# Kernel tuning notes

Hardware: AMD Instinct MI355X
Metric: run time of the kernel (lower is better)

## Reference

```python
import jax, jax.numpy as jnp
import numpy as np

NEG_INF = -1e30
DEN_SCALE = 1.0  # den_scale from init


def segment_logsumexp(scores, segids, num_segments):
    """Numerically stable logsumexp of `scores` grouped by `segids`."""
    m = jax.ops.segment_max(scores, segids, num_segments=num_segments)
    m_safe = jnp.where(m > NEG_INF / 2, m, 0.0)
    s = jax.ops.segment_sum(jnp.exp(scores - m_safe[segids]), segids,
                            num_segments=num_segments)
    return jnp.where(s > 0, jnp.log(s) + m_safe, NEG_INF)


def fsa_log_marginal(ll, seqlen, arc_src, arc_dst, arc_pdf, arc_w,
                     init_logp, final_logp):
    """Forward (alpha) recursion over a compiled FSA.
    ll: [T, C] pdf log-likelihoods; arcs: [A]; states: [S].
    Returns scalar log total path probability."""
    S = init_logp.shape[0]

    def step(carry, ll_t):
        alpha, t = carry
        # score of each arc taken at frame t
        scores = alpha[arc_src] + arc_w + ll_t[arc_pdf]  # [A]
        new_alpha = segment_logsumexp(scores, arc_dst, S)  # [S]
        # freeze alpha once past this sequence's length
        alpha = jnp.where(t < seqlen, new_alpha, alpha)
        return (alpha, t + 1), None

    (alpha, _), _ = jax.lax.scan(step, (init_logp, jnp.array(0, jnp.int32)), ll)
    return jax.nn.logsumexp(alpha + final_logp)


# batched numerator: per-utterance FSA topology ([B, A_num] arc arrays)
_num_marginal = jax.vmap(fsa_log_marginal,
                         in_axes=(0, 0, 0, 0, 0, 0, None, None))
# batched denominator: shared FSA topology ([A_den] arc arrays)
_den_marginal = jax.vmap(fsa_log_marginal,
                         in_axes=(0, 0, None, None, None, None, None, None))


def setup_inputs() -> dict:
    key = jax.random.key(0)
    ks = jax.random.split(key, 10)
    B, T, C = 16, 500, 3000
    S_den, A_den_rand = 2000, 46000
    L = 250  # numerator chain emission length (<= min seqlen)
    S_num = L + 1

    inp = jax.random.normal(ks[0], (B, T, C), dtype=jnp.float32)
    # log-softmax-like normalization, as pdf log-likelihoods would be
    inp = jax.nn.log_softmax(inp, axis=-1)
    seqlengths = jax.random.randint(ks[1], (B,), 300, T + 1).astype(jnp.int32)

    # ---- numerator FSAs: left-to-right chain + self-loops, per utterance ----
    fwd_src = jnp.arange(L, dtype=jnp.int32)            # i -> i+1
    fwd_dst = fwd_src + 1
    loop = jnp.arange(S_num, dtype=jnp.int32)           # self-loops on all states
    num_arc_src = jnp.broadcast_to(jnp.concatenate([fwd_src, loop]), (B, L + S_num))
    num_arc_dst = jnp.broadcast_to(jnp.concatenate([fwd_dst, loop]), (B, L + S_num))
    num_arc_pdf = jax.random.randint(ks[2], (B, L + S_num), 0, C).astype(jnp.int32)
    num_arc_w = jnp.zeros((B, L + S_num), dtype=jnp.float32)
    num_init_logp = jnp.full((S_num,), NEG_INF, jnp.float32).at[0].set(0.0)
    num_final_logp = jnp.full((S_num,), NEG_INF, jnp.float32).at[S_num - 1].set(0.0)

    # ---- denominator FSA: random phone-LM-like graph + self-loops ----
    rnd_src = jax.random.randint(ks[3], (A_den_rand,), 0, S_den)
    rnd_dst = jax.random.randint(ks[4], (A_den_rand,), 0, S_den)
    loops = jnp.arange(S_den)
    den_arc_src = jnp.concatenate([rnd_src, loops]).astype(jnp.int32)
    den_arc_dst = jnp.concatenate([rnd_dst, loops]).astype(jnp.int32)
    A_den = den_arc_src.shape[0]
    den_arc_pdf = jax.random.randint(ks[5], (A_den,), 0, C).astype(jnp.int32)
    den_arc_w = 0.1 * jax.random.normal(ks[6], (A_den,), dtype=jnp.float32)
    den_init_logp = jnp.full((S_den,), NEG_INF, jnp.float32).at[0].set(0.0)
    den_final_logp = jnp.zeros((S_den,), dtype=jnp.float32)

    return {
        "input": inp, "seqlengths": seqlengths,
        "num_arc_src": num_arc_src, "num_arc_dst": num_arc_dst,
        "num_arc_pdf": num_arc_pdf, "num_arc_w": num_arc_w,
        "num_init_logp": num_init_logp, "num_final_logp": num_final_logp,
        "den_arc_src": den_arc_src, "den_arc_dst": den_arc_dst,
        "den_arc_pdf": den_arc_pdf, "den_arc_w": den_arc_w,
        "den_init_logp": den_init_logp, "den_final_logp": den_final_logp,
    }


def reference(input, seqlengths, num_arc_src, num_arc_dst, num_arc_pdf,
              num_arc_w, num_init_logp, num_final_logp, den_arc_src,
              den_arc_dst, den_arc_pdf, den_arc_w, den_init_logp,
              den_final_logp):
    num_llh = _num_marginal(input, seqlengths, num_arc_src, num_arc_dst,
                            num_arc_pdf, num_arc_w, num_init_logp,
                            num_final_logp)
    den_llh = _den_marginal(input, seqlengths, den_arc_src, den_arc_dst,
                            den_arc_pdf, den_arc_w, den_init_logp,
                            den_final_logp)
    loss = -(num_llh - DEN_SCALE * den_llh)
    return loss.sum()
```

## Files before the change

kernel.cpp:

```cpp
#include <hip/hip_runtime.h>

#define NEG_INF_F (-1e30f)
#define MAX_S 2048
#define MAX_C 3008
#define NCH   128

#define VB_SIZE 8216
#define EL_COPY 3016
#define EL_BUF  6032
#define EL_SIZE 12064


__global__ void zero_kernel(int* __restrict__ p, int n) {
  int i = blockIdx.x * blockDim.x + threadIdx.x;
  if (i < n) p[i] = 0;
}

__global__ void hist_kernel(const int* __restrict__ dst, int A, int A_stride,
                            int* __restrict__ cnt, int S) {
  int b = blockIdx.y;
  int i = blockIdx.x * blockDim.x + threadIdx.x;
  if (i < A) atomicAdd(&cnt[b * S + dst[(size_t)b * A_stride + i]], 1);
}

__global__ void hist_chunk_kernel(const int* __restrict__ dst, int A, int chunk, int S,
                                  int* __restrict__ hist) {
  int c = blockIdx.x;
  int i1 = min(A, (c + 1) * chunk);
  for (int i = c * chunk + threadIdx.x; i < i1; i += blockDim.x)
    atomicAdd(&hist[c * S + dst[i]], 1);
}

__global__ void colsum_kernel(const int* __restrict__ hist, int nch, int S,
                              int* __restrict__ cnt) {
  int s = blockIdx.x * blockDim.x + threadIdx.x;
  if (s < S) {
    int t = 0;
    for (int c = 0; c < nch; ++c) t += hist[c * S + s];
    cnt[s] = t;
  }
}

__global__ __launch_bounds__(1024)
void rank_perm_kernel(const int* __restrict__ cnt, int S,
                      int* __restrict__ perm, int* __restrict__ invperm) {
  __shared__ int c[2048];
  __shared__ int R[2048];
  const int tid = threadIdx.x;
  for (int i = tid; i < 2048; i += 1024) c[i] = (i < S) ? cnt[i] : -1;
  __syncthreads();
  for (int u = 0; u < 2; ++u) {
    int s = tid + u * 1024;
    if (s < S) {
      int cs = c[s], r = 0;
      for (int j = 0; j < S; ++j) {
        int cj = c[j];
        r += (cj > cs) || (cj == cs && j < s);
      }
      R[r] = s;
    }
  }
  __syncthreads();
  for (int u = 0; u < 2; ++u) {
    int slot = tid + u * 1024;
    if (slot < S) {
      int state = (slot < 1024) ? R[slot] : R[S - 1 - (slot - 1024)];
      perm[slot] = state;
      invperm[state] = slot;
    }
  }
}

__global__ void pc_kernel(const int* __restrict__ cnt, const int* __restrict__ perm,
                          int S, int* __restrict__ pc) {
  int slot = blockIdx.x * blockDim.x + threadIdx.x;
  if (slot < 2048) pc[slot] = (slot < S) ? ((cnt[perm[slot]] + 3) & ~3) : 0;
}

__global__ void padcnt_kernel(const int* __restrict__ cnt, int n, int* __restrict__ out) {
  int i = blockIdx.x * blockDim.x + threadIdx.x;
  if (i < n) out[i] = (cnt[i] + 3) & ~3;
}

__global__ __launch_bounds__(1024) void scan_kernel(const int* __restrict__ cnt,
                                                    int* __restrict__ rp, int S) {
  __shared__ int buf[2][2048];
  const int tid = threadIdx.x;
  const int b = blockIdx.x;
  const int* c = cnt + (size_t)b * S;
  int* r = rp + (size_t)b * (S + 1);
  for (int u = 0; u < 2; ++u) {
    int i = tid + u * 1024;
    buf[0][i] = (i < S) ? c[i] : 0;
  }
  __syncthreads();
  int cur = 0;
  for (int off = 1; off < 2048; off <<= 1) {
    for (int u = 0; u < 2; ++u) {
      int i = tid + u * 1024;
      buf[cur ^ 1][i] = buf[cur][i] + ((i >= off) ? buf[cur][i - off] : 0);
    }
    __syncthreads();
    cur ^= 1;
  }
  for (int u = 0; u < 2; ++u) {
    int i = tid + u * 1024;
    if (i <= S) r[i] = (i == 0) ? 0 : buf[cur][i - 1];
  }
  if (tid == 0) r[S] = buf[cur][S - 1];
}

__global__ void off_perm_kernel(int* __restrict__ hist, int nch, int S,
                                const int* __restrict__ rp, const int* __restrict__ perm) {
  int slot = blockIdx.x * blockDim.x + threadIdx.x;
  if (slot < S) {
    int state = perm[slot];
    int run = rp[slot];
    for (int c = 0; c < nch; ++c) {
      int h = hist[c * S + state];
      hist[c * S + state] = run;
      run += h;
    }
  }
}

__global__ void pad_den_kernel(const int* __restrict__ rp, const int* __restrict__ cnt,
                               const int* __restrict__ perm, int S, int C,
                               uint2* __restrict__ meta) {
  int slot = blockIdx.x * blockDim.x + threadIdx.x;
  if (slot < S) {
    int p = rp[slot] + cnt[perm[slot]];
    int e = rp[slot + 1];
    const int pc = min(slot, C - 1);
    uint2 pad = make_uint2((unsigned)(slot * 4) | ((unsigned)(pc * 4) << 16), 0u);
    for (; p < e; ++p) meta[p] = pad;
  }
}

__global__ void fill_chunk_kernel(const int* __restrict__ src, const int* __restrict__ dst,
                                  const int* __restrict__ pdf, const float* __restrict__ w,
                                  int A, int chunk, int S, int* __restrict__ hoff,
                                  const int* __restrict__ inv, uint2* __restrict__ meta) {
  int c = blockIdx.y;
  int s = blockIdx.x * blockDim.x + threadIdx.x;
  if (s >= S) return;
  int i1 = min(A, (c + 1) * chunk);
  int p = hoff[c * S + s];
  for (int i = c * chunk; i < i1; ++i) {
    if (dst[i] == s) {
      meta[p++] = make_uint2((unsigned)(inv[src[i]] * 4) | ((unsigned)(pdf[i] * 4) << 16),
                             __float_as_uint(__expf(w[i])));
    }
  }
}

__global__ void fill_kernel(const int* __restrict__ src, const int* __restrict__ dst,
                            const int* __restrict__ pdf, const float* __restrict__ w,
                            int A, int A_stride, const int* __restrict__ rp, int S,
                            uint2* __restrict__ meta, int meta_stride) {
  int b = blockIdx.y;
  int s = blockIdx.x * blockDim.x + threadIdx.x;
  if (s >= S) return;
  const int*   sb = src + (size_t)b * A_stride;
  const int*   db = dst + (size_t)b * A_stride;
  const int*   pb = pdf + (size_t)b * A_stride;
  const float* wb = w   + (size_t)b * A_stride;
  const int*   rpb = rp + (size_t)b * (S + 1);
  uint2* mb = meta + (size_t)b * meta_stride;
  int p = rpb[s];
  for (int i = 0; i < A; ++i) {
    if (db[i] == s) {
      mb[p++] = make_uint2((unsigned)sb[i] | ((unsigned)pb[i] << 16), __float_as_uint(wb[i]));
    }
  }
  uint2 pad = make_uint2(0u, __float_as_uint(NEG_INF_F));
  int e = rpb[s + 1];
  for (; p < e; ++p) mb[p] = pad;
}

__global__ __launch_bounds__(1024)
void wave_desc_kernel(const int* __restrict__ rp, int cap4, int* __restrict__ desc) {
  __shared__ int wm[32];
  const int tid = threadIdx.x;
  const int w = tid >> 6;
  int cA = (rp[tid + 1] - rp[tid]) >> 2;
  int sB = 2047 - tid;
  int cB = (rp[sB + 1] - rp[sB]) >> 2;
  for (int off = 32; off; off >>= 1) {
    cA = max(cA, __shfl_down(cA, off));
    cB = max(cB, __shfl_down(cB, off));
  }
  if ((tid & 63) == 0) { wm[w] = cA; wm[16 + w] = cB; }
  __syncthreads();
  if (tid == 0) {
    int off = 0;
    for (int i = 0; i < 16; ++i) { desc[i] = off; off += wm[i] * 128; }
    for (int i = 0; i < 16; ++i) { desc[16 + i] = off; off += wm[16 + i] * 128; }
    for (int i = 0; i < 16; ++i) { desc[32 + i] = wm[i]; desc[48 + i] = wm[16 + i]; }
    desc[64] = (off <= cap4) ? 1 : 0;
    desc[65] = off;
  }
}

__global__ __launch_bounds__(64)
void repack_choice_kernel(const uint2* __restrict__ meta, const int* __restrict__ rp,
                          const int* __restrict__ desc, int C, uint2* __restrict__ ilv) {
  if (!desc[64]) return;
  const int w = blockIdx.x & 15;
  const bool isB = blockIdx.x >= 16;
  const int l = threadIdx.x;
  const int base4 = desc[(isB ? 16 : 0) + w];
  const int wmax  = desc[(isB ? 48 : 32) + w];
  const int P = wmax * 4;
  if (P == 0) return;

  const int slot_l = isB ? (2047 - (w * 64 + l)) : (w * 64 + l);
  const int r0_l = rp[slot_l];
  const int n_l  = rp[slot_l + 1] - r0_l;
  const int pc_l = min(slot_l, C - 1);
  const uint2 pad_l = make_uint2((unsigned)(slot_l * 4) | ((unsigned)(pc_l * 4) << 16), 0u);

  if (P > 64) {
    const int n4 = n_l >> 2;
    for (int c = 0; c < wmax; ++c) {
      for (int part = 0; part < 2; ++part) {
        int u4 = base4 + c * 128 + part * 64 + l;
        uint2 v0 = pad_l, v1 = pad_l;
        if (c < n4) {
          v0 = meta[r0_l + 4 * c + 2 * part];
          v1 = meta[r0_l + 4 * c + 2 * part + 1];
        }
        ilv[2 * u4]     = v0;
        ilv[2 * u4 + 1] = v1;
      }
    }
    return;
  }

  __shared__ uint2 sp[64][65];

  for (int p = 0; p < P; ++p)
    sp[l][p] = (p < n_l) ? meta[r0_l + p] : pad_l;
  __syncthreads();

  if (l < P) {
    unsigned long long cs[4]  = {0, 0, 0, 0};
    unsigned long long cp2[4] = {0, 0, 0, 0};
    for (int r = 0; r < 64; ++r) {
      uint2 a = sp[r][l];
      unsigned srcoff = a.x & 0xFFFFu;
      unsigned pdfoff = a.x >> 16;
      const int b0 = (int)((srcoff >> 2) & 31u);
      int bestk = 0, bestc = 256;
#pragma unroll
      for (int k = 0; k < 4; ++k) {
        int bb = (b0 + 8 * k) & 31;
        int c = (int)((cs[bb >> 3] >> ((bb & 7) * 8)) & 0xFFull);
        if (c < bestc) { bestc = c; bestk = k; }
      }
      const int bs = (b0 + 8 * bestk) & 31;
      cs[bs >> 3] += (1ULL << ((bs & 7) * 8));
      const int q0 = (int)((pdfoff >> 2) & 31u);
      const int q1 = (q0 + 8) & 31;
      const int c0 = (int)((cp2[q0 >> 3] >> ((q0 & 7) * 8)) & 0xFFull);
      const int c1 = (int)((cp2[q1 >> 3] >> ((q1 & 7) * 8)) & 0xFFull);
      const int bj = (c1 < c0) ? 1 : 0;
      const int qb = bj ? q1 : q0;
      cp2[qb >> 3] += (1ULL << ((qb & 7) * 8));
      a.x = (srcoff + (unsigned)bestk * 8224u) | ((pdfoff + (unsigned)bj * 12064u) << 16);
      sp[r][l] = a;
    }
  }
  __syncthreads();

  for (int c = 0; c < wmax; ++c) {
    for (int part = 0; part < 2; ++part) {
      int u4 = base4 + c * 128 + part * 64 + l;
      ilv[2 * u4]     = sp[l][4 * c + 2 * part];
      ilv[2 * u4 + 1] = sp[l][4 * c + 2 * part + 1];
    }
  }
}


__device__ __forceinline__ float row_lse(const uint2* __restrict__ meta, int k, int e,
                                         const float* __restrict__ alpha,
                                         const float* __restrict__ lcur) {
  float mm0 = NEG_INF_F, ss0 = 0.0f, mm1 = NEG_INF_F, ss1 = 0.0f;
  const int n4 = (e - k) >> 2;
  const uint4* p = (const uint4*)(meta + k);
  if (n4 > 0) {
    uint4 A = p[0], Bv = p[1];
    float t0 = alpha[A.x & 0xFFFFu] + __uint_as_float(A.y) + lcur[A.x >> 16];
    float t1 = alpha[A.z & 0xFFFFu] + __uint_as_float(A.w) + lcur[A.z >> 16];
    float t2 = alpha[Bv.x & 0xFFFFu] + __uint_as_float(Bv.y) + lcur[Bv.x >> 16];
    float t3 = alpha[Bv.z & 0xFFFFu] + __uint_as_float(Bv.w) + lcur[Bv.z >> 16];
    for (int c2 = 1; c2 < n4; ++c2) {
      uint4 A2 = p[2 * c2], B2 = p[2 * c2 + 1];
      float u0 = alpha[A2.x & 0xFFFFu] + __uint_as_float(A2.y) + lcur[A2.x >> 16];
      float u1 = alpha[A2.z & 0xFFFFu] + __uint_as_float(A2.w) + lcur[A2.z >> 16];
      float u2 = alpha[B2.x & 0xFFFFu] + __uint_as_float(B2.y) + lcur[B2.x >> 16];
      float u3 = alpha[B2.z & 0xFFFFu] + __uint_as_float(B2.w) + lcur[B2.z >> 16];
      float mc = fmaxf(fmaxf(t0, t1), fmaxf(t2, t3));
      if ((c2 & 1) != 0) {
        float nm = fmaxf(mm0, mc);
        ss0 = ss0 * __expf(mm0 - nm) +
              ((__expf(t0 - nm) + __expf(t1 - nm)) + (__expf(t2 - nm) + __expf(t3 - nm)));
        mm0 = nm;
      } else {
        float nm = fmaxf(mm1, mc);
        ss1 = ss1 * __expf(mm1 - nm) +
              ((__expf(t0 - nm) + __expf(t1 - nm)) + (__expf(t2 - nm) + __expf(t3 - nm)));
        mm1 = nm;
      }
      t0 = u0; t1 = u1; t2 = u2; t3 = u3;
    }
    float mc = fmaxf(fmaxf(t0, t1), fmaxf(t2, t3));
    if ((n4 & 1) != 0) {
      float nm = fmaxf(mm0, mc);
      ss0 = ss0 * __expf(mm0 - nm) +
            ((__expf(t0 - nm) + __expf(t1 - nm)) + (__expf(t2 - nm) + __expf(t3 - nm)));
      mm0 = nm;
    } else {
      float nm = fmaxf(mm1, mc);
      ss1 = ss1 * __expf(mm1 - nm) +
            ((__expf(t0 - nm) + __expf(t1 - nm)) + (__expf(t2 - nm) + __expf(t3 - nm)));
      mm1 = nm;
    }
  }
  float nm = fmaxf(mm0, mm1);
  float ssc = ss0 * __expf(mm0 - nm) + ss1 * __expf(mm1 - nm);
  return (ssc > 0.0f) ? (__logf(ssc) + nm) : NEG_INF_F;
}

__device__ __forceinline__ void stage_row(const float* __restrict__ row,
                                          float* __restrict__ lds, int C, int tid, int nt) {
  if (((C & 3) == 0) && ((((uintptr_t)row) & 15) == 0)) {
    const float4* r4 = (const float4*)row;
    const int n = C >> 2;
    for (int i = tid; i < n; i += nt) ((float4*)lds)[i] = r4[i];
  } else {
    for (int i = tid; i < C; i += nt) lds[i] = row[i];
  }
}

__device__ __forceinline__ float ldsF(const float* base, unsigned boff) {
  return *(const float*)((const char*)base + boff);
}

#define ACC4(X, Y, s0, s1, s2, s3)                                                         \
  s0 = fmaf(__uint_as_float((X).y), ldsF(vbuf, (X).x & 0xFFFFu) * ldsF(el, (X).x >> 16), s0); \
  s1 = fmaf(__uint_as_float((X).w), ldsF(vbuf, (X).z & 0xFFFFu) * ldsF(el, (X).z >> 16), s1); \
  s2 = fmaf(__uint_as_float((Y).y), ldsF(vbuf, (Y).x & 0xFFFFu) * ldsF(el, (Y).x >> 16), s2); \
  s3 = fmaf(__uint_as_float((Y).w), ldsF(vbuf, (Y).z & 0xFFFFu) * ldsF(el, (Y).z >> 16), s3);

__global__ __launch_bounds__(1024, 1)
void fsa_forward_lin(const float* __restrict__ ll, const int* __restrict__ seqlen,
                     const uint2* __restrict__ den_meta, const uint4* __restrict__ den_ilv,
                     const int* __restrict__ den_desc,
                     const int* __restrict__ den_rp, const int* __restrict__ den_perm, int S_den,
                     const uint2* __restrict__ num_meta, const int* __restrict__ num_rp,
                     int num_stride, int S_num,
                     const float* __restrict__ den_init, const float* __restrict__ den_final,
                     const float* __restrict__ num_init, const float* __restrict__ num_final,
                     int T, int C, int B, float* __restrict__ out_llh)
{
  __shared__ float alpha[MAX_S];
  __shared__ float vbuf[VB_SIZE];
  __shared__ float elbuf[EL_SIZE];
  __shared__ float red[16];
  __shared__ int   sdesc[66];

  const int tid = threadIdx.x;
  const int nt  = 1024;
  const bool is_den = ((int)blockIdx.x) < B;
  const int b = is_den ? (int)blockIdx.x : ((int)blockIdx.x - B);
  const int S = is_den ? S_den : S_num;
  const float* fin  = is_den ? den_final : num_final;
  const int*   perm = is_den ? den_perm  : nullptr;

  const int L = seqlen[b];
  const float* llb = ll + ((size_t)b * T) * C;

  if (is_den) {
    for (int i = tid; i < 66; i += nt) sdesc[i] = den_desc[i];

    const int w = tid >> 6, l = tid & 63;
    const int slotA = tid;
    const int slotB = 2047 - tid;
    const int rA0 = den_rp[slotA], rA1 = den_rp[slotA + 1];
    const int rB0 = den_rp[slotB], rB1 = den_rp[slotB + 1];
    float a0 = (slotA < S) ? den_init[den_perm[slotA]] : NEG_INF_F;
    float a1 = (slotB < S) ? den_init[den_perm[slotB]] : NEG_INF_F;

    const int nvec = C >> 2;
    const bool pf = ((C & 3) == 0) && ((((uintptr_t)llb) & 15) == 0) &&
                    (nvec <= nt) && (C <= MAX_C);

    float lm = fmaxf(a0, a1);
    for (int off = 32; off; off >>= 1) lm = fmaxf(lm, __shfl_down(lm, off));
    if ((tid & 63) == 0) red[tid >> 6] = lm;
    if (L > 0) {
      if (pf) {
        if (tid < nvec) {
          float4 r = ((const float4*)llb)[tid];
          float4 e = make_float4(__expf(r.x), __expf(r.y), __expf(r.z), __expf(r.w));
          ((float4*)elbuf)[tid] = e;
          ((float4*)(elbuf + EL_COPY))[tid] = e;
        }
      } else {
        for (int i = tid; i < C; i += nt) {
          float e = __expf(llb[i]);
          elbuf[i] = e;
          elbuf[i + EL_COPY] = e;
        }
      }
    }
    __syncthreads();
    float M = red[0];
#pragma unroll
    for (int i = 1; i < 16; ++i) M = fmaxf(M, red[i]);

    const bool ilv_ok = sdesc[64] != 0;
    const uint4* pA4 = den_ilv + sdesc[w] + l;
    const uint4* pB4 = den_ilv + sdesc[16 + w] + l;
    const int nA = sdesc[32 + w], nB = sdesc[48 + w];

    int cur = 0;
    for (int t = 0; t < L; ++t) {
      {
        float va = __expf(a0 - M), vb = __expf(a1 - M);
        vbuf[slotA] = va; vbuf[slotA + 2056] = va;
        vbuf[slotA + 4112] = va; vbuf[slotA + 6168] = va;
        vbuf[slotB] = vb; vbuf[slotB + 2056] = vb;
        vbuf[slotB + 4112] = vb; vbuf[slotB + 6168] = vb;
      }
      __syncthreads();

      const float* el = elbuf + (cur ? EL_BUF : 0);

      float4 nx;
      const bool donx = pf && (t + 1 < L) && (tid < nvec);
      if (donx) nx = ((const float4*)(llb + (size_t)(t + 1) * C))[tid];

      float sA0 = 0, sA1 = 0, sA2 = 0, sA3 = 0;
      float sB0 = 0, sB1 = 0, sB2 = 0, sB3 = 0;
      if (ilv_ok) {
        if (nA > 0) {
          uint4 X0 = pA4[0], Y0 = pA4[64];
          if (nA > 1) {
            uint4 X1 = pA4[128], Y1 = pA4[192];
            for (int c = 2; c < nA; ++c) {
              uint4 X2 = pA4[c * 128], Y2 = pA4[c * 128 + 64];
              ACC4(X0, Y0, sA0, sA1, sA2, sA3);
              X0 = X1; Y0 = Y1; X1 = X2; Y1 = Y2;
            }
            ACC4(X0, Y0, sA0, sA1, sA2, sA3);
            X0 = X1; Y0 = Y1;
          }
          ACC4(X0, Y0, sA0, sA1, sA2, sA3);
        }
        if (nB > 0) {
          uint4 X0 = pB4[0], Y0 = pB4[64];
          for (int c = 1; c < nB; ++c) {
            uint4 X1 = pB4[c * 128], Y1 = pB4[c * 128 + 64];
            ACC4(X0, Y0, sB0, sB1, sB2, sB3);
            X0 = X1; Y0 = Y1;
          }
          ACC4(X0, Y0, sB0, sB1, sB2, sB3);
        }
      } else {
        const uint4* pA = (const uint4*)(den_meta + rA0);
        const uint4* pB = (const uint4*)(den_meta + rB0);
        const int nAr = (rA1 - rA0) >> 2, nBr = (rB1 - rB0) >> 2;
        const int n = nAr > nBr ? nAr : nBr;
        for (int c = 0; c < n; ++c) {
          if (c < nAr) {
            uint4 X = pA[2 * c], Y = pA[2 * c + 1];
            ACC4(X, Y, sA0, sA1, sA2, sA3);
          }
          if (c < nBr) {
            uint4 X = pB[2 * c], Y = pB[2 * c + 1];
            ACC4(X, Y, sB0, sB1, sB2, sB3);
          }
        }
      }
      float sA = (sA0 + sA1) + (sA2 + sA3);
      float sB = (sB0 + sB1) + (sB2 + sB3);

      a0 = (sA > 0.0f) ? (__logf(sA) + M) : NEG_INF_F;
      a1 = (sB > 0.0f) ? (__logf(sB) + M) : NEG_INF_F;

      float* eln = elbuf + (cur ? 0 : EL_BUF);
      if (donx) {
        float4 e = make_float4(__expf(nx.x), __expf(nx.y), __expf(nx.z), __expf(nx.w));
        ((float4*)eln)[tid] = e;
        ((float4*)(eln + EL_COPY))[tid] = e;
      } else if (!pf && t + 1 < L) {
        const float* nr = llb + (size_t)(t + 1) * C;
        for (int i = tid; i < C; i += nt) {
          float e = __expf(nr[i]);
          eln[i] = e;
          eln[i + EL_COPY] = e;
        }
      }

      float lm2 = fmaxf(a0, a1);
      for (int off = 32; off; off >>= 1) lm2 = fmaxf(lm2, __shfl_down(lm2, off));
      if ((tid & 63) == 0) red[tid >> 6] = lm2;
      __syncthreads();
      M = red[0];
#pragma unroll
      for (int i = 1; i < 16; ++i) M = fmaxf(M, red[i]);
      cur ^= 1;
    }
    alpha[slotA] = a0;
    alpha[slotB] = a1;
    __syncthreads();
  } else {
    const uint2* meta = num_meta + (size_t)b * num_stride;
    const int*   rp   = num_rp + (size_t)b * (S_num + 1);
    for (int s = tid; s < MAX_S; s += nt) alpha[s] = (s < S) ? num_init[s] : NEG_INF_F;
    int rs[2] = {0, 0}, re[2] = {0, 0};
    for (int u = 0; u < 2; ++u) {
      int s = tid + u * nt;
      if (s < S) { rs[u] = rp[s]; re[u] = rp[s + 1]; }
    }
    __syncthreads();
    for (int t = 0; t < L; ++t) {
      stage_row(llb + (size_t)t * C, elbuf, C, tid, nt);
      __syncthreads();
      float nv[2];
      for (int u = 0; u < 2; ++u) {
        int s = tid + u * nt;
        nv[u] = (s < S) ? row_lse(meta, rs[u], re[u], alpha, elbuf) : NEG_INF_F;
      }
      __syncthreads();
      for (int u = 0; u < 2; ++u) {
        int s = tid + u * nt;
        if (s < S) alpha[s] = nv[u];
      }
      __syncthreads();
    }
  }

  float lm = -3.0e38f;
  for (int s = tid; s < S; s += nt) lm = fmaxf(lm, alpha[s] + fin[perm ? perm[s] : s]);
  for (int off = 32; off; off >>= 1) lm = fmaxf(lm, __shfl_down(lm, off));
  if ((tid & 63) == 0) red[tid >> 6] = lm;
  __syncthreads();
  if (tid < 64) {
    float v = (tid < 16) ? red[tid] : -3.0e38f;
    for (int off = 32; off; off >>= 1) v = fmaxf(v, __shfl_down(v, off));
    if (tid == 0) red[0] = v;
  }
  __syncthreads();
  const float M = red[0];

  float ls = 0.0f;
  for (int s = tid; s < S; s += nt) ls += __expf(alpha[s] + fin[perm ? perm[s] : s] - M);
  for (int off = 32; off; off >>= 1) ls += __shfl_down(ls, off);
  __syncthreads();
  if ((tid & 63) == 0) red[tid >> 6] = ls;
  __syncthreads();
  if (tid < 64) {
    float v = (tid < 16) ? red[tid] : 0.0f;
    for (int off = 32; off; off >>= 1) v += __shfl_down(v, off);
    if (tid == 0) out_llh[(is_den ? 0 : B) + b] = __logf(v) + M;
  }
}


__device__ __forceinline__ unsigned enc_f(float x) {
  unsigned u = __float_as_uint(x);
  return u ^ (unsigned)(((int)u >> 31) | 0x80000000);
}
__device__ __forceinline__ float dec_f(unsigned e) {
  unsigned mask = ((int)e >= 0) ? 0xFFFFFFFFu : 0x80000000u;
  return __uint_as_float(e ^ mask);
}

__global__ __launch_bounds__(1024)
void fsa_forward_fallback(
    const float* __restrict__ ll, const int* __restrict__ seqlen,
    const int* __restrict__ den_src, const int* __restrict__ den_dst,
    const int* __restrict__ den_pdf, const float* __restrict__ den_w,
    int A_den, const float* __restrict__ den_init, const float* __restrict__ den_final, int S_den,
    const int* __restrict__ num_src, const int* __restrict__ num_dst,
    const int* __restrict__ num_pdf, const float* __restrict__ num_w,
    int A_num, const float* __restrict__ num_init, const float* __restrict__ num_final, int S_num,
    int T, int C, int B, float* __restrict__ out_llh)
{
  __shared__ float    alpha[MAX_S];
  __shared__ unsigned menc[MAX_S];
  __shared__ float    msafe[MAX_S];
  __shared__ float    ssum[MAX_S];
  __shared__ float    llrow[MAX_C];

  const int tid = threadIdx.x;
  const int nt  = blockDim.x;
  const bool is_den = ((int)blockIdx.x) < B;
  const int b = is_den ? (int)blockIdx.x : ((int)blockIdx.x - B);
  const int S = is_den ? S_den : S_num;
  const int A = is_den ? A_den : A_num;
  const float* init = is_den ? den_init  : num_init;
  const float* fin  = is_den ? den_final : num_final;
  const int*   asrc = is_den ? den_src  : (num_src + (size_t)b * A_num);
  const int*   adst = is_den ? den_dst  : (num_dst + (size_t)b * A_num);
  const int*   apdf = is_den ? den_pdf  : (num_pdf + (size_t)b * A_num);
  const float* aw   = is_den ? den_w    : (num_w   + (size_t)b * A_num);

  for (int s = tid; s < S; s += nt) { alpha[s] = init[s]; menc[s] = 0u; ssum[s] = 0.0f; }
  __syncthreads();

  const int L = seqlen[b];
  const float* llb = ll + ((size_t)b * T) * C;

  for (int t = 0; t < L; ++t) {
    const float* row = llb + (size_t)t * C;
    for (int i = tid; i < C; i += nt) llrow[i] = row[i];
    __syncthreads();
    for (int i = tid; i < A; i += nt) {
      float score = alpha[asrc[i]] + aw[i] + llrow[apdf[i]];
      atomicMax(&menc[adst[i]], enc_f(score));
    }
    __syncthreads();
    for (int s = tid; s < S; s += nt) {
      float m = dec_f(menc[s]);
      msafe[s] = (m > -5e29f) ? m : 0.0f;
    }
    __syncthreads();
    for (int i = tid; i < A; i += nt) {
      int d = adst[i];
      float score = alpha[asrc[i]] + aw[i] + llrow[apdf[i]];
      atomicAdd(&ssum[d], __expf(score - msafe[d]));
    }
    __syncthreads();
    for (int s = tid; s < S; s += nt) {
      float sum = ssum[s];
      alpha[s] = (sum > 0.0f) ? (__logf(sum) + msafe[s]) : NEG_INF_F;
      menc[s] = 0u; ssum[s] = 0.0f;
    }
    __syncthreads();
  }

  float lm = -3.0e38f;
  for (int s = tid; s < S; s += nt) lm = fmaxf(lm, alpha[s] + fin[s]);
  for (int off = 32; off; off >>= 1) lm = fmaxf(lm, __shfl_down(lm, off));
  const int nwaves = nt >> 6;
  if ((tid & 63) == 0) msafe[tid >> 6] = lm;
  __syncthreads();
  if (tid < 64) {
    float v = (tid < nwaves) ? msafe[tid] : -3.0e38f;
    for (int off = 32; off; off >>= 1) v = fmaxf(v, __shfl_down(v, off));
    if (tid == 0) msafe[MAX_S - 1] = v;
  }
  __syncthreads();
  const float M = msafe[MAX_S - 1];
  float ls = 0.0f;
  for (int s = tid; s < S; s += nt) ls += __expf(alpha[s] + fin[s] - M);
  for (int off = 32; off; off >>= 1) ls += __shfl_down(ls, off);
  if ((tid & 63) == 0) ssum[tid >> 6] = ls;
  __syncthreads();
  if (tid < 64) {
    float v = (tid < nwaves) ? ssum[tid] : 0.0f;
    for (int off = 32; off; off >>= 1) v += __shfl_down(v, off);
    if (tid == 0) out_llh[(is_den ? 0 : B) + b] = __logf(v) + M;
  }
}

__global__ void final_loss_kernel(const float* __restrict__ llh, int B, float* __restrict__ out) {
  int lane = threadIdx.x;
  float v = (lane < B) ? (llh[lane] - llh[B + lane]) : 0.0f;
  for (int off = 32; off; off >>= 1) v += __shfl_down(v, off);
  if (lane == 0) out[0] = v;
}

extern "C" void kernel_launch(void* const* d_in, const int* in_sizes, int n_in,
                              void* d_out, int out_size, void* d_ws, size_t ws_size,
                              hipStream_t stream) {
  const float* ll        = (const float*)d_in[0];
  const int*   seqlen    = (const int*)  d_in[1];
  const int*   num_src   = (const int*)  d_in[2];
  const int*   num_dst   = (const int*)  d_in[3];
  const int*   num_pdf   = (const int*)  d_in[4];
  const float* num_w     = (const float*)d_in[5];
  const float* num_init  = (const float*)d_in[6];
  const float* num_final = (const float*)d_in[7];
  const int*   den_src   = (const int*)  d_in[8];
  const int*   den_dst   = (const int*)  d_in[9];
  const int*   den_pdf   = (const int*)  d_in[10];
  const float* den_w     = (const float*)d_in[11];
  const float* den_init  = (const float*)d_in[12];
  const float* den_final = (const float*)d_in[13];

  const int B     = in_sizes[1];
  const int A_num = in_sizes[2] / B;
  const int S_num = in_sizes[6];
  const int A_den = in_sizes[8];
  const int S_den = in_sizes[12];
  const int T     = 500;
  const int C     = in_sizes[0] / (B * T);

  const int den_cap    = A_den + 3 * S_den + 64;
  const int num_stride = A_num + 3 * S_num + 64;
  const int cap4       = den_cap + 32768;

  size_t off = 0;
  auto alloc = [&](size_t bytes, size_t align) -> size_t {
    off = (off + align - 1) / align * align;
    size_t r = off; off += bytes; return r;
  };
  size_t o_den_meta = alloc((size_t)den_cap * 8, 16);
  size_t o_den_ilv  = alloc((size_t)cap4 * 16, 16);
  size_t o_desc     = alloc((size_t)66 * 4, 4);
  size_t o_num_meta = alloc((size_t)B * num_stride * 8, 16);
  size_t o_den_rp   = alloc((size_t)2049 * 4, 4);
  size_t o_num_rp   = alloc((size_t)B * (S_num + 1) * 4, 4);
  size_t o_den_cnt  = alloc((size_t)S_den * 4, 4);
  size_t o_perm     = alloc((size_t)2048 * 4, 4);
  size_t o_inv      = alloc((size_t)S_den * 4, 4);
  size_t o_pc       = alloc((size_t)2048 * 4, 4);
  size_t o_num_pc   = alloc((size_t)B * S_num * 4, 4);
  size_t o_hist     = alloc((size_t)NCH * S_den * 4, 4);
  size_t o_num_cnt  = alloc((size_t)B * S_num * 4, 4);
  size_t o_llh      = alloc((size_t)2 * B * 4, 4);
  const bool use_csr = (off <= ws_size) && (S_den >= 1) && (S_den <= 2048) &&
                       (S_num >= 1) && (S_num <= 2048) && (C <= MAX_C) && (C >= 1);

  char* wsb = (char*)d_ws;
  float* llh = (float*)(wsb + (use_csr ? o_llh : 0));

  if (use_csr) {
    uint2* den_meta = (uint2*)(wsb + o_den_meta);
    uint4* den_ilv  = (uint4*)(wsb + o_den_ilv);
    int*   desc     = (int*)(wsb + o_desc);
    uint2* num_meta = (uint2*)(wsb + o_num_meta);
    int*   den_rp   = (int*)(wsb + o_den_rp);
    int*   num_rp   = (int*)(wsb + o_num_rp);
    int*   den_cnt  = (int*)(wsb + o_den_cnt);
    int*   perm     = (int*)(wsb + o_perm);
    int*   inv      = (int*)(wsb + o_inv);
    int*   pc       = (int*)(wsb + o_pc);
    int*   num_pc   = (int*)(wsb + o_num_pc);
    int*   hist     = (int*)(wsb + o_hist);
    int*   num_cnt  = (int*)(wsb + o_num_cnt);

    const int chunk = (A_den + NCH - 1) / NCH;

    int ztot = NCH * S_den + B * S_num;
    zero_kernel<<<(ztot + 255) / 256, 256, 0, stream>>>(hist, ztot);

    hist_chunk_kernel<<<NCH, 256, 0, stream>>>(den_dst, A_den, chunk, S_den, hist);
    hist_kernel<<<dim3((A_num + 255) / 256, B), 256, 0, stream>>>(num_dst, A_num, A_num,
                                                                  num_cnt, S_num);

    colsum_kernel<<<(S_den + 255) / 256, 256, 0, stream>>>(hist, NCH, S_den, den_cnt);
    rank_perm_kernel<<<1, 1024, 0, stream>>>(den_cnt, S_den, perm, inv);
    pc_kernel<<<8, 256, 0, stream>>>(den_cnt, perm, S_den, pc);
    scan_kernel<<<1, 1024, 0, stream>>>(pc, den_rp, 2048);
    wave_desc_kernel<<<1, 1024, 0, stream>>>(den_rp, cap4, desc);

    padcnt_kernel<<<(B * S_num + 255) / 256, 256, 0, stream>>>(num_cnt, B * S_num, num_pc);
    scan_kernel<<<B, 1024, 0, stream>>>(num_pc, num_rp, S_num);

    off_perm_kernel<<<(S_den + 255) / 256, 256, 0, stream>>>(hist, NCH, S_den, den_rp, perm);
    pad_den_kernel<<<(S_den + 255) / 256, 256, 0, stream>>>(den_rp, den_cnt, perm, S_den, C,
                                                            den_meta);
    fill_chunk_kernel<<<dim3((S_den + 255) / 256, NCH), 256, 0, stream>>>(
        den_src, den_dst, den_pdf, den_w, A_den, chunk, S_den, hist, inv, den_meta);
    fill_kernel<<<dim3((S_num + 255) / 256, B), 256, 0, stream>>>(
        num_src, num_dst, num_pdf, num_w, A_num, A_num, num_rp, S_num, num_meta, num_stride);

    repack_choice_kernel<<<32, 64, 0, stream>>>(den_meta, den_rp, desc, C, (uint2*)den_ilv);

    fsa_forward_lin<<<2 * B, 1024, 0, stream>>>(
        ll, seqlen, den_meta, den_ilv, desc, den_rp, perm, S_den,
        num_meta, num_rp, num_stride, S_num,
        den_init, den_final, num_init, num_final, T, C, B, llh);
  } else {
    fsa_forward_fallback<<<2 * B, 1024, 0, stream>>>(
        ll, seqlen,
        den_src, den_dst, den_pdf, den_w, A_den, den_init, den_final, S_den,
        num_src, num_dst, num_pdf, num_w, A_num, num_init, num_final, S_num,
        T, C, B, llh);
  }

  final_loss_kernel<<<1, 64, 0, stream>>>(llh, B, (float*)d_out);
}
```

Before: 2.900 ms.

## Fuse graph preprocessing kernels to cut launch count

Merges the denominator histogram, rank/permutation, padded-count scan and wave descriptor steps into one single-block kernel that uses shared-memory atomics. Also fuses the numerator histogram, scan and fill into one per-utterance kernel, and folds zeroing into the chunk histogram. The goal is to remove about ten small kernel launches and their global round trips from the preprocessing chain. The cost is that the denominator histogram now runs serially in a single block over all arcs, and the numerator scan runs on a single thread.

Result: no change. 2.861 ms (-1.3%).

```diff
diff --git a/kernel.cpp b/kernel.cpp
--- a/kernel.cpp
+++ b/kernel.cpp
@@ -11,50 +11,38 @@
 #define EL_SIZE 12064
 
 
-__global__ void zero_kernel(int* __restrict__ p, int n) {
-  int i = blockIdx.x * blockDim.x + threadIdx.x;
-  if (i < n) p[i] = 0;
-}
-
-__global__ void hist_kernel(const int* __restrict__ dst, int A, int A_stride,
-                            int* __restrict__ cnt, int S) {
-  int b = blockIdx.y;
-  int i = blockIdx.x * blockDim.x + threadIdx.x;
-  if (i < A) atomicAdd(&cnt[b * S + dst[(size_t)b * A_stride + i]], 1);
-}
-
 __global__ void hist_chunk_kernel(const int* __restrict__ dst, int A, int chunk, int S,
                                   int* __restrict__ hist) {
-  int c = blockIdx.x;
+  const int c = blockIdx.x;
+  int* h = hist + (size_t)c * S;
+  for (int i = threadIdx.x; i < S; i += blockDim.x) h[i] = 0;
+  __syncthreads();
   int i1 = min(A, (c + 1) * chunk);
   for (int i = c * chunk + threadIdx.x; i < i1; i += blockDim.x)
-    atomicAdd(&hist[c * S + dst[i]], 1);
-}
-
-__global__ void colsum_kernel(const int* __restrict__ hist, int nch, int S,
-                              int* __restrict__ cnt) {
-  int s = blockIdx.x * blockDim.x + threadIdx.x;
-  if (s < S) {
-    int t = 0;
-    for (int c = 0; c < nch; ++c) t += hist[c * S + s];
-    cnt[s] = t;
-  }
+    atomicAdd(&h[dst[i]], 1);
 }
 
 __global__ __launch_bounds__(1024)
-void rank_perm_kernel(const int* __restrict__ cnt, int S,
-                      int* __restrict__ perm, int* __restrict__ invperm) {
-  __shared__ int c[2048];
+void den_stats_kernel(const int* __restrict__ dst, int A, int S, int cap4,
+                      int* __restrict__ rp_g, int* __restrict__ perm_g,
+                      int* __restrict__ inv_g, int* __restrict__ cnt_g,
+                      int* __restrict__ desc) {
+  __shared__ int cnt[2048];
   __shared__ int R[2048];
+  __shared__ int P2[2048];
+  __shared__ int buf[2][2048];
+  __shared__ int wm[32];
   const int tid = threadIdx.x;
-  for (int i = tid; i < 2048; i += 1024) c[i] = (i < S) ? cnt[i] : -1;
+  for (int i = tid; i < 2048; i += 1024) cnt[i] = 0;
+  __syncthreads();
+  for (int i = tid; i < A; i += 1024) atomicAdd(&cnt[dst[i]], 1);
   __syncthreads();
   for (int u = 0; u < 2; ++u) {
     int s = tid + u * 1024;
     if (s < S) {
-      int cs = c[s], r = 0;
+      int cs = cnt[s], r = 0;
       for (int j = 0; j < S; ++j) {
-        int cj = c[j];
+        int cj = cnt[j];
         r += (cj > cs) || (cj == cs && j < s);
       }
       R[r] = s;
@@ -63,36 +51,12 @@
   __syncthreads();
   for (int u = 0; u < 2; ++u) {
     int slot = tid + u * 1024;
-    if (slot < S) {
-      int state = (slot < 1024) ? R[slot] : R[S - 1 - (slot - 1024)];
-      perm[slot] = state;
-      invperm[state] = slot;
-    }
-  }
-}
-
-__global__ void pc_kernel(const int* __restrict__ cnt, const int* __restrict__ perm,
-                          int S, int* __restrict__ pc) {
-  int slot = blockIdx.x * blockDim.x + threadIdx.x;
-  if (slot < 2048) pc[slot] = (slot < S) ? ((cnt[perm[slot]] + 3) & ~3) : 0;
-}
-
-__global__ void padcnt_kernel(const int* __restrict__ cnt, int n, int* __restrict__ out) {
-  int i = blockIdx.x * blockDim.x + threadIdx.x;
-  if (i < n) out[i] = (cnt[i] + 3) & ~3;
-}
-
-__global__ __launch_bounds__(1024) void scan_kernel(const int* __restrict__ cnt,
-                                                    int* __restrict__ rp, int S) {
-  __shared__ int buf[2][2048];
-  const int tid = threadIdx.x;
-  const int b = blockIdx.x;
-  const int* c = cnt + (size_t)b * S;
-  int* r = rp + (size_t)b * (S + 1);
-  for (int u = 0; u < 2; ++u) {
-    int i = tid + u * 1024;
-    buf[0][i] = (i < S) ? c[i] : 0;
-  }
+    int state = (slot < S) ? ((slot < 1024) ? R[slot] : R[S - 1 - (slot - 1024)]) : -1;
+    P2[slot] = state;
+    if (slot < S) { perm_g[slot] = state; inv_g[state] = slot; }
+    buf[0][slot] = (slot < S) ? ((cnt[state] + 3) & ~3) : 0;
+  }
+  for (int i = tid; i < S; i += 1024) cnt_g[i] = cnt[i];
   __syncthreads();
   int cur = 0;
   for (int off = 1; off < 2048; off <<= 1) {
@@ -105,36 +69,45 @@
   }
   for (int u = 0; u < 2; ++u) {
     int i = tid + u * 1024;
-    if (i <= S) r[i] = (i == 0) ? 0 : buf[cur][i - 1];
-  }
-  if (tid == 0) r[S] = buf[cur][S - 1];
-}
-
-__global__ void off_perm_kernel(int* __restrict__ hist, int nch, int S,
-                                const int* __restrict__ rp, const int* __restrict__ perm) {
+    rp_g[i] = (i == 0) ? 0 : buf[cur][i - 1];
+  }
+  if (tid == 0) rp_g[2048] = buf[cur][2047];
+  int cA = ((P2[tid] >= 0) ? ((cnt[P2[tid]] + 3) & ~3) : 0) >> 2;
+  const int sB = 2047 - tid;
+  int cB = ((P2[sB] >= 0) ? ((cnt[P2[sB]] + 3) & ~3) : 0) >> 2;
+  for (int off = 32; off; off >>= 1) {
+    cA = max(cA, __shfl_down(cA, off));
+    cB = max(cB, __shfl_down(cB, off));
+  }
+  if ((tid & 63) == 0) { wm[tid >> 6] = cA; wm[16 + (tid >> 6)] = cB; }
+  __syncthreads();
+  if (tid == 0) {
+    int off = 0;
+    for (int i = 0; i < 16; ++i) { desc[i] = off; off += wm[i] * 128; }
+    for (int i = 0; i < 16; ++i) { desc[16 + i] = off; off += wm[16 + i] * 128; }
+    for (int i = 0; i < 16; ++i) { desc[32 + i] = wm[i]; desc[48 + i] = wm[16 + i]; }
+    desc[64] = (off <= cap4) ? 1 : 0;
+    desc[65] = off;
+  }
+}
+
+__global__ void offpad_kernel(int* __restrict__ hist, int nch, int S,
+                              const int* __restrict__ rp, const int* __restrict__ perm,
+                              const int* __restrict__ cnt, int C, uint2* __restrict__ meta) {
   int slot = blockIdx.x * blockDim.x + threadIdx.x;
-  if (slot < S) {
-    int state = perm[slot];
-    int run = rp[slot];
-    for (int c = 0; c < nch; ++c) {
-      int h = hist[c * S + state];
-      hist[c * S + state] = run;
-      run += h;
-    }
-  }
-}
-
-__global__ void pad_den_kernel(const int* __restrict__ rp, const int* __restrict__ cnt,
-                               const int* __restrict__ perm, int S, int C,
-                               uint2* __restrict__ meta) {
-  int slot = blockIdx.x * blockDim.x + threadIdx.x;
-  if (slot < S) {
-    int p = rp[slot] + cnt[perm[slot]];
-    int e = rp[slot + 1];
-    const int pc = min(slot, C - 1);
-    uint2 pad = make_uint2((unsigned)(slot * 4) | ((unsigned)(pc * 4) << 16), 0u);
-    for (; p < e; ++p) meta[p] = pad;
-  }
+  if (slot >= S) return;
+  int state = perm[slot];
+  int run = rp[slot];
+  for (int c = 0; c < nch; ++c) {
+    int h = hist[c * S + state];
+    hist[c * S + state] = run;
+    run += h;
+  }
+  int p = rp[slot] + cnt[state];
+  int e = rp[slot + 1];
+  const int pc = min(slot, C - 1);
+  uint2 pad = make_uint2((unsigned)(slot * 4) | ((unsigned)(pc * 4) << 16), 0u);
+  for (; p < e; ++p) meta[p] = pad;
 }
 
 __global__ void fill_chunk_kernel(const int* __restrict__ src, const int* __restrict__ dst,
@@ -154,51 +127,41 @@
   }
 }
 
-__global__ void fill_kernel(const int* __restrict__ src, const int* __restrict__ dst,
-                            const int* __restrict__ pdf, const float* __restrict__ w,
-                            int A, int A_stride, const int* __restrict__ rp, int S,
-                            uint2* __restrict__ meta, int meta_stride) {
-  int b = blockIdx.y;
-  int s = blockIdx.x * blockDim.x + threadIdx.x;
-  if (s >= S) return;
-  const int*   sb = src + (size_t)b * A_stride;
-  const int*   db = dst + (size_t)b * A_stride;
-  const int*   pb = pdf + (size_t)b * A_stride;
-  const float* wb = w   + (size_t)b * A_stride;
-  const int*   rpb = rp + (size_t)b * (S + 1);
+__global__ __launch_bounds__(256)
+void num_build_kernel(const int* __restrict__ src, const int* __restrict__ dst,
+                      const int* __restrict__ pdf, const float* __restrict__ w,
+                      int A, int S, int* __restrict__ rp_g,
+                      uint2* __restrict__ meta, int meta_stride) {
+  __shared__ int cnt[2048];
+  __shared__ int rp[2049];
+  const int b = blockIdx.x;
+  const int tid = threadIdx.x;
+  const int*   sb = src + (size_t)b * A;
+  const int*   db = dst + (size_t)b * A;
+  const int*   pb = pdf + (size_t)b * A;
+  const float* wb = w   + (size_t)b * A;
   uint2* mb = meta + (size_t)b * meta_stride;
-  int p = rpb[s];
-  for (int i = 0; i < A; ++i) {
-    if (db[i] == s) {
-      mb[p++] = make_uint2((unsigned)sb[i] | ((unsigned)pb[i] << 16), __float_as_uint(wb[i]));
-    }
-  }
-  uint2 pad = make_uint2(0u, __float_as_uint(NEG_INF_F));
-  int e = rpb[s + 1];
-  for (; p < e; ++p) mb[p] = pad;
-}
-
-__global__ __launch_bounds__(1024)
-void wave_desc_kernel(const int* __restrict__ rp, int cap4, int* __restrict__ desc) {
-  __shared__ int wm[32];
-  const int tid = threadIdx.x;
-  const int w = tid >> 6;
-  int cA = (rp[tid + 1] - rp[tid]) >> 2;
-  int sB = 2047 - tid;
-  int cB = (rp[sB + 1] - rp[sB]) >> 2;
-  for (int off = 32; off; off >>= 1) {
-    cA = max(cA, __shfl_down(cA, off));
-    cB = max(cB, __shfl_down(cB, off));
-  }
-  if ((tid & 63) == 0) { wm[w] = cA; wm[16 + w] = cB; }
+  for (int i = tid; i < S; i += 256) cnt[i] = 0;
+  __syncthreads();
+  for (int i = tid; i < A; i += 256) atomicAdd(&cnt[db[i]], 1);
   __syncthreads();
   if (tid == 0) {
-    int off = 0;
-    for (int i = 0; i < 16; ++i) { desc[i] = off; off += wm[i] * 128; }
-    for (int i = 0; i < 16; ++i) { desc[16 + i] = off; off += wm[16 + i] * 128; }
-    for (int i = 0; i < 16; ++i) { desc[32 + i] = wm[i]; desc[48 + i] = wm[16 + i]; }
-    desc[64] = (off <= cap4) ? 1 : 0;
-    desc[65] = off;
+    int run = 0;
+    for (int s = 0; s < S; ++s) { rp[s] = run; run += (cnt[s] + 3) & ~3; }
+    rp[S] = run;
+  }
+  __syncthreads();
+  for (int i = tid; i <= S; i += 256) rp_g[(size_t)b * (S + 1) + i] = rp[i];
+  const uint2 pad = make_uint2(0u, __float_as_uint(NEG_INF_F));
+  for (int s = tid; s < S; s += 256) {
+    int p = rp[s];
+    for (int i = 0; i < A; ++i) {
+      if (db[i] == s) {
+        mb[p++] = make_uint2((unsigned)sb[i] | ((unsigned)pb[i] << 16),
+                             __float_as_uint(wb[i]));
+      }
+    }
+    for (int e = rp[s + 1]; p < e; ++p) mb[p] = pad;
   }
 }
 
@@ -720,10 +683,7 @@
   size_t o_den_cnt  = alloc((size_t)S_den * 4, 4);
   size_t o_perm     = alloc((size_t)2048 * 4, 4);
   size_t o_inv      = alloc((size_t)S_den * 4, 4);
-  size_t o_pc       = alloc((size_t)2048 * 4, 4);
-  size_t o_num_pc   = alloc((size_t)B * S_num * 4, 4);
   size_t o_hist     = alloc((size_t)NCH * S_den * 4, 4);
-  size_t o_num_cnt  = alloc((size_t)B * S_num * 4, 4);
   size_t o_llh      = alloc((size_t)2 * B * 4, 4);
   const bool use_csr = (off <= ws_size) && (S_den >= 1) && (S_den <= 2048) &&
                        (S_num >= 1) && (S_num <= 2048) && (C <= MAX_C) && (C >= 1);
@@ -741,37 +701,19 @@
     int*   den_cnt  = (int*)(wsb + o_den_cnt);
     int*   perm     = (int*)(wsb + o_perm);
     int*   inv      = (int*)(wsb + o_inv);
-    int*   pc       = (int*)(wsb + o_pc);
-    int*   num_pc   = (int*)(wsb + o_num_pc);
     int*   hist     = (int*)(wsb + o_hist);
-    int*   num_cnt  = (int*)(wsb + o_num_cnt);
 
     const int chunk = (A_den + NCH - 1) / NCH;
 
-    int ztot = NCH * S_den + B * S_num;
-    zero_kernel<<<(ztot + 255) / 256, 256, 0, stream>>>(hist, ztot);
-
     hist_chunk_kernel<<<NCH, 256, 0, stream>>>(den_dst, A_den, chunk, S_den, hist);
-    hist_kernel<<<dim3((A_num + 255) / 256, B), 256, 0, stream>>>(num_dst, A_num, A_num,
-                                                                  num_cnt, S_num);
-
-    colsum_kernel<<<(S_den + 255) / 256, 256, 0, stream>>>(hist, NCH, S_den, den_cnt);
-    rank_perm_kernel<<<1, 1024, 0, stream>>>(den_cnt, S_den, perm, inv);
-    pc_kernel<<<8, 256, 0, stream>>>(den_cnt, perm, S_den, pc);
-    scan_kernel<<<1, 1024, 0, stream>>>(pc, den_rp, 2048);
-    wave_desc_kernel<<<1, 1024, 0, stream>>>(den_rp, cap4, desc);
-
-    padcnt_kernel<<<(B * S_num + 255) / 256, 256, 0, stream>>>(num_cnt, B * S_num, num_pc);
-    scan_kernel<<<B, 1024, 0, stream>>>(num_pc, num_rp, S_num);
-
-    off_perm_kernel<<<(S_den + 255) / 256, 256, 0, stream>>>(hist, NCH, S_den, den_rp, perm);
-    pad_den_kernel<<<(S_den + 255) / 256, 256, 0, stream>>>(den_rp, den_cnt, perm, S_den, C,
-                                                            den_meta);
+    den_stats_kernel<<<1, 1024, 0, stream>>>(den_dst, A_den, S_den, cap4,
+                                             den_rp, perm, inv, den_cnt, desc);
+    offpad_kernel<<<(S_den + 255) / 256, 256, 0, stream>>>(hist, NCH, S_den, den_rp, perm,
+                                                           den_cnt, C, den_meta);
     fill_chunk_kernel<<<dim3((S_den + 255) / 256, NCH), 256, 0, stream>>>(
         den_src, den_dst, den_pdf, den_w, A_den, chunk, S_den, hist, inv, den_meta);
-    fill_kernel<<<dim3((S_num + 255) / 256, B), 256, 0, stream>>>(
-        num_src, num_dst, num_pdf, num_w, A_num, A_num, num_rp, S_num, num_meta, num_stride);
-
+    num_build_kernel<<<B, 256, 0, stream>>>(num_src, num_dst, num_pdf, num_w,
+                                            A_num, S_num, num_rp, num_meta, num_stride);
     repack_choice_kernel<<<32, 64, 0, stream>>>(den_meta, den_rp, desc, C, (uint2*)den_ilv);
 
     fsa_forward_lin<<<2 * B, 1024, 0, stream>>>(
```
